# Optimization experiments

Measured on AMD Instinct MI355X. Metric: run time of the kernel, lower is better.

Reference implementation:

```python
import jax, jax.numpy as jnp
import numpy as np

L, D, H, DH, DF = 4, 512, 8, 64, 2048
B, S = 4, 2048
EPS = 1e-6  # fast-transformers causal-linear eps


def _ln(x, g, b, eps=1e-5):
    mu = jnp.mean(x, axis=-1, keepdims=True)
    var = jnp.var(x, axis=-1, keepdims=True)
    return (x - mu) * jax.lax.rsqrt(var + eps) * g + b


def _causal_linear(Q, K, V):
    # Q, K, V: [B, S, H, DH]; O(N) linear-attention recurrence over S
    Qs = jnp.moveaxis(Q, 1, 0)
    Ks = jnp.moveaxis(K, 1, 0)
    Vs = jnp.moveaxis(V, 1, 0)
    b = Q.shape[0]
    kv0 = jnp.zeros((b, H, DH, DH), Q.dtype)  # running sum of k v^T
    z0 = jnp.zeros((b, H, DH), Q.dtype)       # running sum of k

    def step(carry, qkv):
        kv, z = carry
        q, k, v = qkv  # each [B, H, DH]
        kv = kv + k[..., :, None] * v[..., None, :]
        z = z + k
        num = jnp.einsum('bhd,bhdm->bhm', q, kv)
        den = jnp.einsum('bhd,bhd->bh', q, z) + EPS
        return (kv, z), num / den[..., None]

    _, out = jax.lax.scan(step, (kv0, z0), (Qs, Ks, Vs))
    return jnp.moveaxis(out, 0, 1)  # [B, S, H, DH]


def _layer(x, p):
    Wq, bq, Wk, bk, Wv, bv, Wo, bo, W1, b1, W2, b2, g1, be1, g2, be2 = p
    b, s, _ = x.shape
    q = (x @ Wq + bq).reshape(b, s, H, DH)
    k = (x @ Wk + bk).reshape(b, s, H, DH)
    v = (x @ Wv + bv).reshape(b, s, H, DH)
    Qf = jax.nn.elu(q) + 1.0  # feature map phi(x) = elu(x) + 1
    Kf = jax.nn.elu(k) + 1.0
    a = _causal_linear(Qf, Kf, v).reshape(b, s, D)
    x = x + (a @ Wo + bo)            # residual (dropout=0)
    x = _ln(x, g1, be1)              # post-norm
    y = jax.nn.gelu(x @ W1 + b1, approximate=False) @ W2 + b2
    return _ln(x + y, g2, be2)


def _encoder(h, params, gf, bef):
    def body(x, p):
        return _layer(x, p), None
    x, _ = jax.lax.scan(body, h, params)
    return _ln(x, gf, bef)  # final LayerNorm from builder


def setup_inputs() -> dict:
    key = jax.random.key(0)
    ks = jax.random.split(key, 8)

    def w(k, shape, fan_in):
        return jax.random.normal(k, shape, jnp.float32) * (fan_in ** -0.5)

    return {
        'h': jax.random.normal(ks[0], (B, S, D), jnp.float32),
        'Wq': w(ks[1], (L, D, D), D), 'bq': jnp.zeros((L, D), jnp.float32),
        'Wk': w(ks[2], (L, D, D), D), 'bk': jnp.zeros((L, D), jnp.float32),
        'Wv': w(ks[3], (L, D, D), D), 'bv': jnp.zeros((L, D), jnp.float32),
        'Wo': w(ks[4], (L, D, D), D), 'bo': jnp.zeros((L, D), jnp.float32),
        'W1': w(ks[5], (L, D, DF), D), 'b1': jnp.zeros((L, DF), jnp.float32),
        'W2': w(ks[6], (L, DF, D), DF), 'b2': jnp.zeros((L, D), jnp.float32),
        'g1': jnp.ones((L, D), jnp.float32), 'be1': jnp.zeros((L, D), jnp.float32),
        'g2': jnp.ones((L, D), jnp.float32), 'be2': jnp.zeros((L, D), jnp.float32),
        'gf': jnp.ones((D,), jnp.float32), 'bef': jnp.zeros((D,), jnp.float32),
    }


def reference(h, Wq, bq, Wk, bk, Wv, bv, Wo, bo, W1, b1, W2, b2,
              g1, be1, g2, be2, gf, bef):
    params = (Wq, bq, Wk, bk, Wv, bv, Wo, bo, W1, b1, W2, b2, g1, be1, g2, be2)
    return _encoder(h, params, gf, bef)
```

## Files before the change

### kernel.cpp

```cpp
#include <hip/hip_runtime.h>
#include <hip/hip_bf16.h>
#include <math.h>

#define LAYERS 4
#define DMODEL 512
#define NH 8
#define DH 64
#define DFF 2048
#define NB 4
#define S_LEN 2048
#define MROWS 8192
#define CHUNK 64
#define NCHUNK 32
#define ATT_EPS 1e-6f
#define LN_EPS 1e-5f
#define SEGSTRIDE (MROWS * DMODEL)

typedef __attribute__((ext_vector_type(8))) short short8v;
typedef __attribute__((ext_vector_type(4))) float f32x4;

__device__ __forceinline__ float b2f(unsigned short u) {
    union { float f; unsigned u; } c; c.u = ((unsigned)u) << 16; return c.f;
}
__device__ __forceinline__ unsigned short f2b(float f) {
    union { float f; unsigned u; } c; c.f = f;
    unsigned r = c.u + 0x7FFFu + ((c.u >> 16) & 1u);
    return (unsigned short)(r >> 16);
}
__device__ __forceinline__ void gload16(const void* g, void* l) {
    __builtin_amdgcn_global_load_lds(
        (const __attribute__((address_space(1))) void*)g,
        (__attribute__((address_space(3))) void*)l, 16, 0, 0);
}
__device__ __forceinline__ float elu1f(float v) {
    return (v > 0.f) ? (v + 1.f) : __expf(v);
}
__device__ __forceinline__ float geluf(float v) {
    float u = 0.7978845608028654f * v * (1.f + 0.044715f * v * v);
    float th = 1.f - 2.f / (1.f + __expf(2.f * u));
    return 0.5f * v * (1.f + th);
}

template <int ACT>
__global__ __launch_bounds__(512, 4) void gemmw(
    const unsigned short* __restrict__ A,
    const unsigned short* __restrict__ WT,
    const float* __restrict__ b0, const float* __restrict__ b1,
    const float* __restrict__ b2,
    unsigned short* __restrict__ Cbf,
    int M, int N, int K)
{
    __shared__ short S[2][12288];

    const int t = threadIdx.x;
    const int m0 = blockIdx.x * 128, n0 = blockIdx.y * 256;
    const int lane = t & 63, wid = t >> 6;
    const int wm = (wid >> 2) * 64;
    const int wn = (wid & 3) * 64;
    const int fr = lane & 15, kg = lane >> 4;

    const unsigned short* gA;
    const unsigned short* gB0;
    const unsigned short* gB1;
    int loA, loB0, loB1;
    {
        const int rowA = t >> 2, spA = t & 3;
        gA = A + (size_t)(m0 + rowA) * K + (spA ^ ((rowA >> 1) & 3)) * 8;
        loA = t * 8;
        const int rB0 = t >> 2, sB0 = t & 3;
        gB0 = WT + (size_t)(n0 + rB0) * K + (sB0 ^ ((rB0 >> 1) & 3)) * 8;
        loB0 = 4096 + t * 8;
        const int u1 = t + 512;
        const int rB1 = u1 >> 2, sB1 = u1 & 3;
        gB1 = WT + (size_t)(n0 + rB1) * K + (sB1 ^ ((rB1 >> 1) & 3)) * 8;
        loB1 = 4096 + u1 * 8;
    }

    int aoff[4], boff[4];
#pragma unroll
    for (int m = 0; m < 4; ++m) {
        const int R = wm + m * 16 + fr;
        aoff[m] = R * 32 + ((kg ^ ((R >> 1) & 3)) << 3);
    }
#pragma unroll
    for (int n = 0; n < 4; ++n) {
        const int R = wn + n * 16 + fr;
        boff[n] = 4096 + R * 32 + ((kg ^ ((R >> 1) & 3)) << 3);
    }

    f32x4 acc[4][4];
#pragma unroll
    for (int m = 0; m < 4; ++m)
#pragma unroll
        for (int n = 0; n < 4; ++n) acc[m][n] = (f32x4){0.f, 0.f, 0.f, 0.f};

#define STAGE(b, kt) do {                                       \
    gload16(gA + (size_t)(kt) * 32, &S[b][loA]);                \
    gload16(gB0 + (size_t)(kt) * 32, &S[b][loB0]);              \
    gload16(gB1 + (size_t)(kt) * 32, &S[b][loB1]); } while (0)

    const int NT = K >> 5;
    STAGE(0, 0);

    for (int td = 0; td < NT; ++td) {
        const int b = td & 1;
        if (td + 1 < NT) {
            STAGE(b ^ 1, td + 1);
            __builtin_amdgcn_sched_barrier(0);
            asm volatile("s_waitcnt vmcnt(3)");
        } else {
            __builtin_amdgcn_sched_barrier(0);
            asm volatile("s_waitcnt vmcnt(0)");
        }
        __builtin_amdgcn_sched_barrier(0);
        __builtin_amdgcn_s_barrier();
        __builtin_amdgcn_sched_barrier(0);

        short8v af[4], bf[4];
#pragma unroll
        for (int m = 0; m < 4; ++m) af[m] = *(const short8v*)&S[b][aoff[m]];
#pragma unroll
        for (int n = 0; n < 4; ++n) bf[n] = *(const short8v*)&S[b][boff[n]];

        asm volatile("s_waitcnt lgkmcnt(0)");
        __builtin_amdgcn_sched_barrier(0);
        __builtin_amdgcn_s_setprio(1);
#pragma unroll
        for (int m = 0; m < 4; ++m)
#pragma unroll
            for (int n = 0; n < 4; ++n)
                acc[m][n] = __builtin_amdgcn_mfma_f32_16x16x32_bf16(
                    af[m], bf[n], acc[m][n], 0, 0, 0);
        __builtin_amdgcn_s_setprio(0);

        __builtin_amdgcn_sched_barrier(0);
        __builtin_amdgcn_s_barrier();
    }
#undef STAGE

    const int seg = (ACT == 3) ? (n0 >> 9) : 0;
    const float* bias = (ACT == 3) ? (seg == 0 ? b0 : (seg == 1 ? b1 : b2)) : b0;
    float bv[4];
#pragma unroll
    for (int n = 0; n < 4; ++n) {
        const int col = n0 + wn + n * 16 + fr;
        bv[n] = bias[(ACT == 3) ? (col - seg * 512) : col];
    }

#pragma unroll
    for (int m = 0; m < 4; ++m)
#pragma unroll
        for (int n = 0; n < 4; ++n)
#pragma unroll
            for (int j = 0; j < 4; ++j) {
                const int row = m0 + wm + m * 16 + (lane >> 4) * 4 + j;
                const int col = n0 + wn + n * 16 + fr;
                float v = acc[m][n][j] + bv[n];
                if (ACT == 2) v = geluf(v);
                else if (ACT == 3) { if (seg < 2) v = elu1f(v); }
                if (ACT == 3)
                    Cbf[(size_t)seg * SEGSTRIDE + (size_t)row * 512 + (col - seg * 512)] = f2b(v);
                else
                    Cbf[(size_t)row * N + col] = f2b(v);
            }
}

template <int ACT, bool RESID, bool ATOMIC, bool WU, bool WBF16, int KSPLIT>
__global__ __launch_bounds__(512, 4) void gemm8(
    const unsigned short* __restrict__ A,
    const unsigned short* __restrict__ WT,
    const float* __restrict__ b0,
    const unsigned short* __restrict__ Xres,
    float* __restrict__ U, unsigned short* __restrict__ Cbf,
    int M, int N, int K)
{
    __shared__ short S[2][16384];

    const int t = threadIdx.x;
    const int m0 = blockIdx.x * 128, n0 = blockIdx.y * 128;
    const int kz = (KSPLIT > 1) ? blockIdx.z : 0;
    const int Kc = K / KSPLIT;
    const int kbeg = kz * Kc;
    const int lane = t & 63, wid = t >> 6;
    const int wm = (wid >> 2) * 64;
    const int wn = (wid & 3) * 32;
    const int fr = lane & 15, kg = lane >> 4;

    const unsigned short* gsrc[4];
    int ldso[4];
#pragma unroll
    for (int r = 0; r < 4; ++r) {
        const int u = (r & 1) ? (t + 512) : t;
        const bool isA = (r < 2);
        const int row = u >> 3, sp = u & 7, sl = sp ^ (row & 7);
        gsrc[r] = (isA ? A + (size_t)(m0 + row) * K
                       : WT + (size_t)(n0 + row) * K) + kbeg + sl * 8;
        ldso[r] = (isA ? 0 : 8192) + u * 8;
    }

    int aoff[2][4], boff[2][2];
#pragma unroll
    for (int h = 0; h < 2; ++h) {
#pragma unroll
        for (int m = 0; m < 4; ++m) {
            const int R = wm + m * 16 + fr;
            aoff[h][m] = R * 64 + (((h * 4 + kg) ^ (R & 7)) * 8);
        }
#pragma unroll
        for (int n = 0; n < 2; ++n) {
            const int R = wn + n * 16 + fr;
            boff[h][n] = 8192 + R * 64 + (((h * 4 + kg) ^ (R & 7)) * 8);
        }
    }

    f32x4 acc[4][2];
#pragma unroll
    for (int m = 0; m < 4; ++m)
#pragma unroll
        for (int n = 0; n < 2; ++n) acc[m][n] = (f32x4){0.f, 0.f, 0.f, 0.f};

#define STAGE(b, kt) do { _Pragma("unroll")                                  \
    for (int r = 0; r < 4; ++r)                                              \
        gload16(gsrc[r] + (size_t)(kt) * 64, &S[b][ldso[r]]); } while (0)

    const int NT = Kc >> 6;
    STAGE(0, 0);

    for (int td = 0; td < NT; ++td) {
        const int b = td & 1;
        if (td + 1 < NT) {
            STAGE(b ^ 1, td + 1);
            __builtin_amdgcn_sched_barrier(0);
            asm volatile("s_waitcnt vmcnt(4)");
        } else {
            __builtin_amdgcn_sched_barrier(0);
            asm volatile("s_waitcnt vmcnt(0)");
        }
        __builtin_amdgcn_sched_barrier(0);
        __builtin_amdgcn_s_barrier();
        __builtin_amdgcn_sched_barrier(0);

        short8v a0[4], b0f[2], a1[4], b1f[2];
#pragma unroll
        for (int m = 0; m < 4; ++m) a0[m] = *(const short8v*)&S[b][aoff[0][m]];
#pragma unroll
        for (int n = 0; n < 2; ++n) b0f[n] = *(const short8v*)&S[b][boff[0][n]];
#pragma unroll
        for (int m = 0; m < 4; ++m) a1[m] = *(const short8v*)&S[b][aoff[1][m]];
#pragma unroll
        for (int n = 0; n < 2; ++n) b1f[n] = *(const short8v*)&S[b][boff[1][n]];

        asm volatile("s_waitcnt lgkmcnt(6)");
        __builtin_amdgcn_sched_barrier(0);
        __builtin_amdgcn_s_setprio(1);
#pragma unroll
        for (int m = 0; m < 4; ++m)
#pragma unroll
            for (int n = 0; n < 2; ++n)
                acc[m][n] = __builtin_amdgcn_mfma_f32_16x16x32_bf16(
                    a0[m], b0f[n], acc[m][n], 0, 0, 0);
        __builtin_amdgcn_s_setprio(0);

        asm volatile("s_waitcnt lgkmcnt(0)");
        __builtin_amdgcn_sched_barrier(0);
        __builtin_amdgcn_s_setprio(1);
#pragma unroll
        for (int m = 0; m < 4; ++m)
#pragma unroll
            for (int n = 0; n < 2; ++n)
                acc[m][n] = __builtin_amdgcn_mfma_f32_16x16x32_bf16(
                    a1[m], b1f[n], acc[m][n], 0, 0, 0);
        __builtin_amdgcn_s_setprio(0);

        __builtin_amdgcn_sched_barrier(0);
        __builtin_amdgcn_s_barrier();
    }
#undef STAGE

    float bv[2];
#pragma unroll
    for (int n = 0; n < 2; ++n)
        bv[n] = b0[n0 + wn + n * 16 + fr];
    if (KSPLIT > 1 && kz != 0) { bv[0] = 0.f; bv[1] = 0.f; }

#pragma unroll
    for (int m = 0; m < 4; ++m)
#pragma unroll
        for (int n = 0; n < 2; ++n)
#pragma unroll
            for (int j = 0; j < 4; ++j) {
                const int row = m0 + wm + m * 16 + (lane >> 4) * 4 + j;
                const int col = n0 + wn + n * 16 + fr;
                float v = acc[m][n][j] + bv[n];
                if (RESID && kz == 0)
                    v += b2f(Xres[(size_t)row * 512 + col]);
                if (ACT == 1) v = elu1f(v);
                else if (ACT == 2) v = geluf(v);
                if (ATOMIC) {
                    atomicAdd(&U[(size_t)row * N + col], v);
                } else if (WU) {
                    U[(size_t)row * N + col] = v;
                }
                if (WBF16)
                    Cbf[(size_t)row * N + col] = f2b(v);
            }
}

__global__ __launch_bounds__(256) void transpose_to_bf16(
    const float* __restrict__ W, unsigned short* __restrict__ WT, int K, int N,
    size_t wstride, size_t tstride)
{
    __shared__ float tile[32][33];
    const int l = blockIdx.z;
    W += (size_t)l * wstride;
    WT += (size_t)l * tstride;
    const int k0 = blockIdx.x * 32, n0 = blockIdx.y * 32;
    const int tx = threadIdx.x & 31, ty = threadIdx.x >> 5;
#pragma unroll
    for (int i = ty; i < 32; i += 8)
        tile[i][tx] = W[(size_t)(k0 + i) * N + n0 + tx];
    __syncthreads();
#pragma unroll
    for (int i = ty; i < 32; i += 8)
        WT[(size_t)(n0 + i) * K + k0 + tx] = f2b(tile[tx][i]);
}

__global__ __launch_bounds__(256) void cvt_in(
    const float* __restrict__ h, unsigned short* __restrict__ xb, int n)
{
    const int i = (blockIdx.x * 256 + threadIdx.x) * 8;
    if (i >= n) return;
    f32x4 a = *(const f32x4*)(h + i);
    f32x4 b = *(const f32x4*)(h + i + 4);
    short8v p;
    p[0] = f2b(a[0]); p[1] = f2b(a[1]); p[2] = f2b(a[2]); p[3] = f2b(a[3]);
    p[4] = f2b(b[0]); p[5] = f2b(b[1]); p[6] = f2b(b[2]); p[7] = f2b(b[3]);
    *(short8v*)(xb + i) = p;
}

__device__ __forceinline__ int swzo(int row, int sl) {
    return row * 64 + ((sl ^ (row & 7)) << 3);
}

__global__ __launch_bounds__(256) void attn_stage1(
    const unsigned short* __restrict__ Kf, const unsigned short* __restrict__ Vf,
    unsigned short* __restrict__ KVp, float* __restrict__ zp)
{
    const int c = blockIdx.x, hh = blockIdx.y, bb = blockIdx.z;
    const int t = threadIdx.x;
    const int lane = t & 63, w = t >> 6;
    const int fr = lane & 15, g = lane >> 4;

    __shared__ unsigned short KTs[64 * 72];
    __shared__ unsigned short VTs[64 * 72];

    const size_t rowbase = (size_t)(bb * S_LEN + c * CHUNK);
    const int colbase = hh * DH;

    {
        const int r = lane, cs = w * 16;
        const unsigned short* kp = Kf + (rowbase + r) * DMODEL + colbase + cs;
        const unsigned short* vp = Vf + (rowbase + r) * DMODEL + colbase + cs;
        short8v k0 = *(const short8v*)kp, k1 = *(const short8v*)(kp + 8);
        short8v v0 = *(const short8v*)vp, v1 = *(const short8v*)(vp + 8);
#pragma unroll
        for (int i = 0; i < 8; ++i) {
            KTs[(cs + i) * 72 + r]     = (unsigned short)k0[i];
            KTs[(cs + 8 + i) * 72 + r] = (unsigned short)k1[i];
            VTs[(cs + i) * 72 + r]     = (unsigned short)v0[i];
            VTs[(cs + 8 + i) * 72 + r] = (unsigned short)v1[i];
        }
    }
    __syncthreads();

    f32x4 cacc[4];
#pragma unroll
    for (int nf = 0; nf < 4; ++nf) cacc[nf] = (f32x4){0.f, 0.f, 0.f, 0.f};

    const short8v a0 = *(const short8v*)&VTs[(w * 16 + fr) * 72 + g * 8];
    const short8v a1 = *(const short8v*)&VTs[(w * 16 + fr) * 72 + (4 + g) * 8];
#pragma unroll
    for (int nf = 0; nf < 4; ++nf) {
        short8v bq0 = *(const short8v*)&KTs[(nf * 16 + fr) * 72 + g * 8];
        short8v bq1 = *(const short8v*)&KTs[(nf * 16 + fr) * 72 + (4 + g) * 8];
        cacc[nf] = __builtin_amdgcn_mfma_f32_16x16x32_bf16(a0, bq0, cacc[nf], 0, 0, 0);
        cacc[nf] = __builtin_amdgcn_mfma_f32_16x16x32_bf16(a1, bq1, cacc[nf], 0, 0, 0);
    }

    const size_t base = ((size_t)(bb * NH + hh) * NCHUNK + c) * (DH * DH);
#pragma unroll
    for (int nf = 0; nf < 4; ++nf)
#pragma unroll
        for (int reg = 0; reg < 4; ++reg) {
            const int e = w * 16 + g * 4 + reg;
            const int d = nf * 16 + fr;
            KVp[base + e * 64 + d] = f2b(cacc[nf][reg]);
        }

    if (t < 64) {
        float s = 0.f;
#pragma unroll
        for (int sl = 0; sl < 8; ++sl) {
            short8v kv = *(const short8v*)&KTs[t * 72 + sl * 8];
#pragma unroll
            for (int i = 0; i < 8; ++i) s += b2f((unsigned short)kv[i]);
        }
        zp[((size_t)(bb * NH + hh) * NCHUNK + c) * DH + t] = s;
    }
}

__global__ __launch_bounds__(256) void attn_stage2(
    const unsigned short* __restrict__ KVp, unsigned short* __restrict__ KVb,
    float* __restrict__ zp)
{
    const int bh = blockIdx.x;
    const int e = blockIdx.y * 256 + threadIdx.x;
    const size_t base = (size_t)bh * NCHUNK * (DH * DH) + e;
    float run = 0.f;
#pragma unroll 4
    for (int c = 0; c < NCHUNK; ++c) {
        const float tmp = b2f(KVp[base + (size_t)c * (DH * DH)]);
        KVb[base + (size_t)c * (DH * DH)] = f2b(run);
        run += tmp;
    }
    if (blockIdx.y == 0 && threadIdx.x < DH) {
        float rz = 0.f;
        const size_t zb = (size_t)bh * NCHUNK * DH + threadIdx.x;
#pragma unroll 4
        for (int c = 0; c < NCHUNK; ++c) {
            const float tmp = zp[zb + c * DH];
            zp[zb + c * DH] = rz;
            rz += tmp;
        }
    }
}

__global__ __launch_bounds__(256) void attn_stage3(
    const unsigned short* __restrict__ Qf, const unsigned short* __restrict__ Kf,
    const unsigned short* __restrict__ Vf, const unsigned short* __restrict__ KVb,
    const float* __restrict__ zp, unsigned short* __restrict__ Af)
{
    const int c = blockIdx.x, hh = blockIdx.y, bb = blockIdx.z;
    const int t = threadIdx.x;
    const int lane = t & 63, w = t >> 6;
    const int fr = lane & 15, g = lane >> 4;

    __shared__ unsigned short Qs[4096];
    __shared__ unsigned short Ks[4096];
    __shared__ unsigned short KVts[4096];
    __shared__ unsigned short VTs[64 * 72];
    __shared__ unsigned short Ps[64 * 72];
    __shared__ float zsh[DH];
    __shared__ float den_lds[64];

    const size_t rowbase = (size_t)(bb * S_LEN + c * CHUNK);
    const int colbase = hh * DH;
    const size_t kvbase = ((size_t)(bb * NH + hh) * NCHUNK + c) * (DH * DH);

#pragma unroll
    for (int iss = 0; iss < 2; ++iss) {
        const int u = iss * 256 + t, row = u >> 3, sl = u & 7;
        const int ssl = (sl ^ (row & 7)) * 8;
        gload16(Qf + (rowbase + row) * DMODEL + colbase + ssl, &Qs[(size_t)u * 8]);
        gload16(Kf + (rowbase + row) * DMODEL + colbase + ssl, &Ks[(size_t)u * 8]);
        gload16(KVb + kvbase + row * 64 + ssl, &KVts[(size_t)u * 8]);
    }
    {
        const int r = lane, cs = w * 16;
        const unsigned short* vp = Vf + (rowbase + r) * DMODEL + colbase + cs;
        short8v v0 = *(const short8v*)vp, v1 = *(const short8v*)(vp + 8);
#pragma unroll
        for (int i = 0; i < 8; ++i) {
            VTs[(cs + i) * 72 + r]     = (unsigned short)v0[i];
            VTs[(cs + 8 + i) * 72 + r] = (unsigned short)v1[i];
        }
    }
    if (t < DH) zsh[t] = zp[((size_t)(bb * NH + hh) * NCHUNK + c) * DH + t];
    __syncthreads();

    f32x4 c1[4];
#pragma unroll
    for (int mf = 0; mf < 4; ++mf) c1[mf] = (f32x4){0.f, 0.f, 0.f, 0.f};
    {
        const short8v bq0 = *(const short8v*)&Qs[swzo(w * 16 + fr, g)];
        const short8v bq1 = *(const short8v*)&Qs[swzo(w * 16 + fr, 4 + g)];
#pragma unroll
        for (int mf = 0; mf < 4; ++mf) {
            short8v ak0 = *(const short8v*)&Ks[swzo(mf * 16 + fr, g)];
            short8v ak1 = *(const short8v*)&Ks[swzo(mf * 16 + fr, 4 + g)];
            c1[mf] = __builtin_amdgcn_mfma_f32_16x16x32_bf16(ak0, bq0, c1[mf], 0, 0, 0);
            c1[mf] = __builtin_amdgcn_mfma_f32_16x16x32_bf16(ak1, bq1, c1[mf], 0, 0, 0);
        }
    }

    const int i_my = w * 16 + fr;
    float dint = 0.f;
#pragma unroll
    for (int mf = 0; mf < 4; ++mf)
#pragma unroll
        for (int reg = 0; reg < 4; ++reg) {
            const int j = mf * 16 + g * 4 + reg;
            const float v = (j <= i_my) ? c1[mf][reg] : 0.f;
            dint += v;
            Ps[i_my * 72 + j] = f2b(v);
        }
    dint += __shfl_xor(dint, 16);
    dint += __shfl_xor(dint, 32);

    float dpre = 0.f;
#pragma unroll
    for (int sl = 0; sl < 8; ++sl) {
        short8v qv = *(const short8v*)&Qs[swzo(i_my, sl)];
#pragma unroll
        for (int e = 0; e < 8; ++e) dpre += b2f((unsigned short)qv[e]) * zsh[sl * 8 + e];
    }
    if (g == 0) den_lds[i_my] = dpre + dint + ATT_EPS;

    f32x4 acc[4];
#pragma unroll
    for (int nf = 0; nf < 4; ++nf) acc[nf] = (f32x4){0.f, 0.f, 0.f, 0.f};
    {
        const short8v aq0 = *(const short8v*)&Qs[swzo(w * 16 + fr, g)];
        const short8v aq1 = *(const short8v*)&Qs[swzo(w * 16 + fr, 4 + g)];
#pragma unroll
        for (int nf = 0; nf < 4; ++nf) {
            short8v bkv0 = *(const short8v*)&KVts[swzo(nf * 16 + fr, g)];
            short8v bkv1 = *(const short8v*)&KVts[swzo(nf * 16 + fr, 4 + g)];
            acc[nf] = __builtin_amdgcn_mfma_f32_16x16x32_bf16(aq0, bkv0, acc[nf], 0, 0, 0);
            acc[nf] = __builtin_amdgcn_mfma_f32_16x16x32_bf16(aq1, bkv1, acc[nf], 0, 0, 0);
        }
        const short8v ap0 = *(const short8v*)&Ps[(w * 16 + fr) * 72 + g * 8];
        const short8v ap1 = *(const short8v*)&Ps[(w * 16 + fr) * 72 + (4 + g) * 8];
#pragma unroll
        for (int nf = 0; nf < 4; ++nf) {
            short8v bv0 = *(const short8v*)&VTs[(nf * 16 + fr) * 72 + g * 8];
            short8v bv1 = *(const short8v*)&VTs[(nf * 16 + fr) * 72 + (4 + g) * 8];
            acc[nf] = __builtin_amdgcn_mfma_f32_16x16x32_bf16(ap0, bv0, acc[nf], 0, 0, 0);
            acc[nf] = __builtin_amdgcn_mfma_f32_16x16x32_bf16(ap1, bv1, acc[nf], 0, 0, 0);
        }
    }

#pragma unroll
    for (int reg = 0; reg < 4; ++reg) {
        const int i = w * 16 + g * 4 + reg;
        const float inv = 1.f / den_lds[i];
        unsigned short* dst = Af + (rowbase + i) * DMODEL + colbase;
#pragma unroll
        for (int nf = 0; nf < 4; ++nf)
            dst[nf * 16 + fr] = f2b(acc[nf][reg] * inv);
    }
}

__global__ __launch_bounds__(256) void ln_u2x(float* __restrict__ U,
                                              const float* __restrict__ g,
                                              const float* __restrict__ b,
                                              unsigned short* __restrict__ Xb,
                                              int ZERO)
{
    const size_t row = blockIdx.x * 4 + (threadIdx.x >> 6);
    const int t = threadIdx.x & 63;
    float* ur = U + row * DMODEL;
    f32x4 x0 = *(const f32x4*)&ur[t * 4];
    f32x4 x1 = *(const f32x4*)&ur[256 + t * 4];

    float s  = x0[0] + x0[1] + x0[2] + x0[3] + x1[0] + x1[1] + x1[2] + x1[3];
    float sq = x0[0]*x0[0] + x0[1]*x0[1] + x0[2]*x0[2] + x0[3]*x0[3] +
               x1[0]*x1[0] + x1[1]*x1[1] + x1[2]*x1[2] + x1[3]*x1[3];
#pragma unroll
    for (int m = 1; m < 64; m <<= 1) {
        s  += __shfl_xor(s, m);
        sq += __shfl_xor(sq, m);
    }
    const float mu  = s * (1.f / DMODEL);
    const float var = sq * (1.f / DMODEL) - mu * mu;
    const float rr  = rsqrtf(var + LN_EPS);

    const int c0 = t * 4, c1 = 256 + t * 4;
    f32x4 g0 = *(const f32x4*)&g[c0], g1v = *(const f32x4*)&g[c1];
    f32x4 b0 = *(const f32x4*)&b[c0], b1v = *(const f32x4*)&b[c1];
    unsigned short* xb = Xb + row * DMODEL;
    ushort4 u0, u1;
    u0.x = f2b((x0[0] - mu) * rr * g0[0] + b0[0]);
    u0.y = f2b((x0[1] - mu) * rr * g0[1] + b0[1]);
    u0.z = f2b((x0[2] - mu) * rr * g0[2] + b0[2]);
    u0.w = f2b((x0[3] - mu) * rr * g0[3] + b0[3]);
    u1.x = f2b((x1[0] - mu) * rr * g1v[0] + b1v[0]);
    u1.y = f2b((x1[1] - mu) * rr * g1v[1] + b1v[1]);
    u1.z = f2b((x1[2] - mu) * rr * g1v[2] + b1v[2]);
    u1.w = f2b((x1[3] - mu) * rr * g1v[3] + b1v[3]);
    *(ushort4*)&xb[c0] = u0;
    *(ushort4*)&xb[c1] = u1;
    if (ZERO) {
        *(f32x4*)&ur[c0] = (f32x4){0.f, 0.f, 0.f, 0.f};
        *(f32x4*)&ur[c1] = (f32x4){0.f, 0.f, 0.f, 0.f};
    }
}

__global__ __launch_bounds__(256) void ln_final(const unsigned short* __restrict__ Xb,
                                                const float* __restrict__ g,
                                                const float* __restrict__ b,
                                                float* __restrict__ Out)
{
    const size_t row = blockIdx.x * 4 + (threadIdx.x >> 6);
    const int t = threadIdx.x & 63;
    const unsigned short* xr = Xb + row * DMODEL;
    short8v xv = *(const short8v*)&xr[t * 8];
    float x[8];
#pragma unroll
    for (int i = 0; i < 8; ++i) x[i] = b2f((unsigned short)xv[i]);

    float s = 0.f, sq = 0.f;
#pragma unroll
    for (int i = 0; i < 8; ++i) { s += x[i]; sq += x[i] * x[i]; }
#pragma unroll
    for (int m = 1; m < 64; m <<= 1) {
        s  += __shfl_xor(s, m);
        sq += __shfl_xor(sq, m);
    }
    const float mu  = s * (1.f / DMODEL);
    const float var = sq * (1.f / DMODEL) - mu * mu;
    const float rr  = rsqrtf(var + LN_EPS);

    float* orow = Out + row * DMODEL + t * 8;
    f32x4 o0, o1;
#pragma unroll
    for (int i = 0; i < 4; ++i) {
        o0[i] = (x[i] - mu) * rr * g[t * 8 + i] + b[t * 8 + i];
        o1[i] = (x[4 + i] - mu) * rr * g[t * 8 + 4 + i] + b[t * 8 + 4 + i];
    }
    *(f32x4*)orow = o0;
    *(f32x4*)(orow + 4) = o1;
}

extern "C" void kernel_launch(void* const* d_in, const int* in_sizes, int n_in,
                              void* d_out, int out_size, void* d_ws, size_t ws_size,
                              hipStream_t stream)
{
    const float* h   = (const float*)d_in[0];
    const float* Wq  = (const float*)d_in[1];
    const float* bq  = (const float*)d_in[2];
    const float* Wk  = (const float*)d_in[3];
    const float* bk  = (const float*)d_in[4];
    const float* Wv  = (const float*)d_in[5];
    const float* bv  = (const float*)d_in[6];
    const float* Wo  = (const float*)d_in[7];
    const float* bo  = (const float*)d_in[8];
    const float* W1  = (const float*)d_in[9];
    const float* b1  = (const float*)d_in[10];
    const float* W2  = (const float*)d_in[11];
    const float* b2  = (const float*)d_in[12];
    const float* g1  = (const float*)d_in[13];
    const float* be1 = (const float*)d_in[14];
    const float* g2  = (const float*)d_in[15];
    const float* be2 = (const float*)d_in[16];
    const float* gf  = (const float*)d_in[17];
    const float* bef = (const float*)d_in[18];

    char* ws = (char*)d_ws;
    const size_t MB = 1024 * 1024;
    unsigned short* x_bf = (unsigned short*)(ws);
    unsigned short* qkv  = (unsigned short*)(ws + 8 * MB);
    unsigned short* qb   = qkv;
    unsigned short* kb   = qkv + SEGSTRIDE;
    unsigned short* vb   = qkv + 2 * (size_t)SEGSTRIDE;
    unsigned short* ab   = (unsigned short*)(ws + 32 * MB);
    unsigned short* hid  = (unsigned short*)(ws + 8 * MB);
    unsigned short* KVp  = (unsigned short*)(ws + 40 * MB);
    unsigned short* KVb  = (unsigned short*)(ws + 48 * MB);
    float* U             = (float*)(ws + 40 * MB);
    float* zp            = (float*)(ws + 56 * MB);
    unsigned short* WTall = (unsigned short*)(ws + 57 * MB);

    const int M = MROWS, D = DMODEL, DF = DFF;
    const size_t LSTR = 3 * 1024 * 1024;

    cvt_in<<<dim3(M * D / (256 * 8)), 256, 0, stream>>>(h, x_bf, M * D);
    transpose_to_bf16<<<dim3(D / 32, D / 32, LAYERS), 256, 0, stream>>>(
        Wq, WTall, D, D, (size_t)D * D, LSTR);
    transpose_to_bf16<<<dim3(D / 32, D / 32, LAYERS), 256, 0, stream>>>(
        Wk, WTall + 262144, D, D, (size_t)D * D, LSTR);
    transpose_to_bf16<<<dim3(D / 32, D / 32, LAYERS), 256, 0, stream>>>(
        Wv, WTall + 524288, D, D, (size_t)D * D, LSTR);
    transpose_to_bf16<<<dim3(D / 32, D / 32, LAYERS), 256, 0, stream>>>(
        Wo, WTall + 786432, D, D, (size_t)D * D, LSTR);
    transpose_to_bf16<<<dim3(D / 32, DF / 32, LAYERS), 256, 0, stream>>>(
        W1, WTall + 1048576, D, DF, (size_t)D * DF, LSTR);
    transpose_to_bf16<<<dim3(DF / 32, D / 32, LAYERS), 256, 0, stream>>>(
        W2, WTall + 2097152, DF, D, (size_t)DF * D, LSTR);

    for (int l = 0; l < LAYERS; ++l) {
        unsigned short* WL = WTall + (size_t)l * LSTR;
        const unsigned short* WqkvT = WL;
        const unsigned short* WoT   = WL + 786432;
        const unsigned short* W1T   = WL + 1048576;
        const unsigned short* W2T   = WL + 2097152;

        gemmw<3><<<dim3(M / 128, 1536 / 256), 512, 0, stream>>>(
            x_bf, WqkvT, bq + (size_t)l * D, bk + (size_t)l * D, bv + (size_t)l * D,
            qkv, M, 1536, D);

        attn_stage1<<<dim3(NCHUNK, NH, NB), 256, 0, stream>>>(kb, vb, KVp, zp);
        attn_stage2<<<dim3(NB * NH, 16), 256, 0, stream>>>(KVp, KVb, zp);
        attn_stage3<<<dim3(NCHUNK, NH, NB), 256, 0, stream>>>(qb, kb, vb, KVb, zp, ab);

        gemm8<0, true, false, true, false, 1>
            <<<dim3(M / 128, D / 128), 512, 0, stream>>>(
            ab, WoT, bo + (size_t)l * D, x_bf, U, nullptr, M, D, D);
        ln_u2x<<<dim3(M / 4), 256, 0, stream>>>(U, g1 + (size_t)l * D, be1 + (size_t)l * D, x_bf, 1);

        gemmw<2><<<dim3(M / 128, DF / 256), 512, 0, stream>>>(
            x_bf, W1T, b1 + (size_t)l * DF, nullptr, nullptr, hid, M, DF, D);
        gemm8<0, true, true, false, false, 2>
            <<<dim3(M / 128, D / 128, 2), 512, 0, stream>>>(
            hid, W2T, b2 + (size_t)l * D, x_bf, U, nullptr, M, D, DF);
        ln_u2x<<<dim3(M / 4), 256, 0, stream>>>(U, g2 + (size_t)l * D, be2 + (size_t)l * D, x_bf, 0);
    }

    ln_final<<<dim3(M / 4), 256, 0, stream>>>(x_bf, gf, bef, (float*)d_out);
}
```

Baseline: 601.0 us.

## Replace atomic split-K reduction with bf16 partial buffers summed in LayerNorm

The W2 split-K GEMM now writes each K-half's partial result as bf16 to separate segments instead of doing fp32 atomicAdd into a zeroed buffer. A new LayerNorm kernel sums the two partials before normalizing, so the zeroing pass in the first LayerNorm is removed. The W1 GEMM also moves from the wide gemmw kernel to gemm8 with 128-wide tiles. This trades atomic traffic and fp32 bandwidth for bf16 rounding of the partial sums, which adds some precision error.

Measured after the change: 536.1 us, median of 2. 10.8% less time.

```diff
diff --git a/kernel.cpp b/kernel.cpp
--- a/kernel.cpp
+++ b/kernel.cpp
@@ -165,7 +165,7 @@
             }
 }
 
-template <int ACT, bool RESID, bool ATOMIC, bool WU, bool WBF16, int KSPLIT>
+template <int ACT, bool RESID, bool WU, bool WBF16, int KSPLIT>
 __global__ __launch_bounds__(512, 4) void gemm8(
     const unsigned short* __restrict__ A,
     const unsigned short* __restrict__ WT,
@@ -296,13 +296,14 @@
                     v += b2f(Xres[(size_t)row * 512 + col]);
                 if (ACT == 1) v = elu1f(v);
                 else if (ACT == 2) v = geluf(v);
-                if (ATOMIC) {
-                    atomicAdd(&U[(size_t)row * N + col], v);
-                } else if (WU) {
+                if (WU)
                     U[(size_t)row * N + col] = v;
+                if (WBF16) {
+                    if (KSPLIT > 1)
+                        Cbf[(size_t)kz * SEGSTRIDE + (size_t)row * N + col] = f2b(v);
+                    else
+                        Cbf[(size_t)row * N + col] = f2b(v);
                 }
-                if (WBF16)
-                    Cbf[(size_t)row * N + col] = f2b(v);
             }
 }
 
@@ -551,15 +552,14 @@
     }
 }
 
-__global__ __launch_bounds__(256) void ln_u2x(float* __restrict__ U,
+__global__ __launch_bounds__(256) void ln_u2x(const float* __restrict__ U,
                                               const float* __restrict__ g,
                                               const float* __restrict__ b,
-                                              unsigned short* __restrict__ Xb,
-                                              int ZERO)
+                                              unsigned short* __restrict__ Xb)
 {
     const size_t row = blockIdx.x * 4 + (threadIdx.x >> 6);
     const int t = threadIdx.x & 63;
-    float* ur = U + row * DMODEL;
+    const float* ur = U + row * DMODEL;
     f32x4 x0 = *(const f32x4*)&ur[t * 4];
     f32x4 x1 = *(const f32x4*)&ur[256 + t * 4];
 
@@ -590,10 +590,41 @@
     u1.w = f2b((x1[3] - mu) * rr * g1v[3] + b1v[3]);
     *(ushort4*)&xb[c0] = u0;
     *(ushort4*)&xb[c1] = u1;
-    if (ZERO) {
-        *(f32x4*)&ur[c0] = (f32x4){0.f, 0.f, 0.f, 0.f};
-        *(f32x4*)&ur[c1] = (f32x4){0.f, 0.f, 0.f, 0.f};
-    }
+}
+
+__global__ __launch_bounds__(256) void ln_2b(const unsigned short* __restrict__ U0b,
+                                             const unsigned short* __restrict__ U1b,
+                                             const float* __restrict__ g,
+                                             const float* __restrict__ b,
+                                             unsigned short* __restrict__ Xb)
+{
+    const size_t row = blockIdx.x * 4 + (threadIdx.x >> 6);
+    const int t = threadIdx.x & 63;
+    short8v v0 = *(const short8v*)&U0b[row * DMODEL + t * 8];
+    short8v v1 = *(const short8v*)&U1b[row * DMODEL + t * 8];
+    float x[8];
+#pragma unroll
+    for (int i = 0; i < 8; ++i)
+        x[i] = b2f((unsigned short)v0[i]) + b2f((unsigned short)v1[i]);
+
+    float s = 0.f, sq = 0.f;
+#pragma unroll
+    for (int i = 0; i < 8; ++i) { s += x[i]; sq += x[i] * x[i]; }
+#pragma unroll
+    for (int m = 1; m < 64; m <<= 1) {
+        s  += __shfl_xor(s, m);
+        sq += __shfl_xor(sq, m);
+    }
+    const float mu  = s * (1.f / DMODEL);
+    const float var = sq * (1.f / DMODEL) - mu * mu;
+    const float rr  = rsqrtf(var + LN_EPS);
+
+    unsigned short* xb = Xb + row * DMODEL + t * 8;
+    short8v p;
+#pragma unroll
+    for (int i = 0; i < 8; ++i)
+        p[i] = f2b((x[i] - mu) * rr * g[t * 8 + i] + b[t * 8 + i]);
+    *(short8v*)xb = p;
 }
 
 __global__ __launch_bounds__(256) void ln_final(const unsigned short* __restrict__ Xb,
@@ -668,6 +699,7 @@
     unsigned short* KVp  = (unsigned short*)(ws + 40 * MB);
     unsigned short* KVb  = (unsigned short*)(ws + 48 * MB);
     float* U             = (float*)(ws + 40 * MB);
+    unsigned short* U01b = (unsigned short*)(ws + 40 * MB);
     float* zp            = (float*)(ws + 56 * MB);
     unsigned short* WTall = (unsigned short*)(ws + 57 * MB);
 
@@ -703,17 +735,19 @@
         attn_stage2<<<dim3(NB * NH, 16), 256, 0, stream>>>(KVp, KVb, zp);
         attn_stage3<<<dim3(NCHUNK, NH, NB), 256, 0, stream>>>(qb, kb, vb, KVb, zp, ab);
 
-        gemm8<0, true, false, true, false, 1>
+        gemm8<0, true, true, false, 1>
             <<<dim3(M / 128, D / 128), 512, 0, stream>>>(
             ab, WoT, bo + (size_t)l * D, x_bf, U, nullptr, M, D, D);
-        ln_u2x<<<dim3(M / 4), 256, 0, stream>>>(U, g1 + (size_t)l * D, be1 + (size_t)l * D, x_bf, 1);
-
-        gemmw<2><<<dim3(M / 128, DF / 256), 512, 0, stream>>>(
+        ln_u2x<<<dim3(M / 4), 256, 0, stream>>>(U, g1 + (size_t)l * D, be1 + (size_t)l * D, x_bf);
+
+        gemm8<2, false, false, true, 1>
+            <<<dim3(M / 128, DF / 128), 512, 0, stream>>>(
             x_bf, W1T, b1 + (size_t)l * DF, nullptr, nullptr, hid, M, DF, D);
-        gemm8<0, true, true, false, false, 2>
+        gemm8<0, true, false, true, 2>
             <<<dim3(M / 128, D / 128, 2), 512, 0, stream>>>(
-            hid, W2T, b2 + (size_t)l * D, x_bf, U, nullptr, M, D, DF);
-        ln_u2x<<<dim3(M / 4), 256, 0, stream>>>(U, g2 + (size_t)l * D, be2 + (size_t)l * D, x_bf, 0);
+            hid, W2T, b2 + (size_t)l * D, x_bf, nullptr, U01b, M, D, DF);
+        ln_2b<<<dim3(M / 4), 256, 0, stream>>>(U01b, U01b + SEGSTRIDE,
+            g2 + (size_t)l * D, be2 + (size_t)l * D, x_bf);
     }
 
     ln_final<<<dim3(M / 4), 256, 0, stream>>>(x_bf, gf, bef, (float*)d_out);
```
